# Kernel tuning notes

Hardware: AMD Instinct MI355X
Metric: run time of the kernel (lower is better)

## Reference

```python
import jax, jax.numpy as jnp
import numpy as np

CONTEXT = 256   # context_size
INITIAL = 32    # initial_size
HIDDEN = 256    # hidden_size
WINDOW = 64 - 1 # module stores window_size - 1
TEMP = 50000.0  # soft-argmax temperature
MAX_STEPS = CONTEXT - INITIAL  # cur_pt >= 1 guarantees >=1 index advance per step
B = 4096


def setup_inputs() -> dict:
    key = jax.random.key(0)
    ks = jax.random.split(key, 4)
    def lin_w(k, fan_in, fan_out):
        bound = 1.0 / np.sqrt(fan_in)
        return jax.random.uniform(k, (fan_in, fan_out), jnp.float32, -bound, bound)
    return {
        "x": jax.random.normal(ks[0], (B, CONTEXT), jnp.float32),
        "hid_W": lin_w(ks[1], HIDDEN, HIDDEN),
        "hid_b": jnp.zeros((HIDDEN,), jnp.float32),
        "in_W": lin_w(ks[2], INITIAL, HIDDEN),
        "in_b": jnp.zeros((HIDDEN,), jnp.float32),
        "pred_W": lin_w(ks[3], HIDDEN, WINDOW),
        "pred_b": jnp.zeros((WINDOW,), jnp.float32),
    }


def reference(x, hid_W, hid_b, in_W, in_b, pred_W, pred_b):
    # with per-item active masks. Padded/dense outputs:
    #   pts  [B, MAX_STEPS] : predicted change points (last point dropped, rest zero-padded)
    #   mx   [B, CONTEXT]   : all sigmoid-masked slices scattered back to their positions
    # returned concatenated as [B, MAX_STEPS + CONTEXT].
    Bv = x.shape[0]
    rows = jnp.arange(Bv)[:, None]
    jW = jnp.arange(WINDOW, dtype=jnp.float32)
    iI = jnp.arange(INITIAL)
    iWin = jnp.arange(WINDOW)

    def step(carry, _):
        last, hidden, masked_x, count = carry
        active = last < CONTEXT                       # torch: skip items whose last pt >= context
        last_long = last.astype(jnp.int32)            # floor (last >= INITIAL > 0)
        # slice x[i, last-INITIAL : last]; first step last=INITIAL -> x[:, 0:INITIAL]
        idx = last_long[:, None] - INITIAL + iI       # [B, I]
        slices = jnp.take_along_axis(x, idx, axis=1)
        new_hidden = jnp.tanh(hidden @ hid_W + hid_b + slices @ in_W + in_b)
        hidden = jnp.where(active[:, None], new_hidden, hidden)
        w = new_hidden @ pred_W + pred_b              # [B, WINDOW]
        p = jax.nn.softmax(w * TEMP, axis=-1)
        cur_pt = jnp.minimum(p @ jW + 1.0, float(WINDOW))        # soft-argmax + 1, clamped
        seq_end = jnp.minimum(cur_pt + last, float(CONTEXT))
        seq_end_long = seq_end.astype(jnp.int32)
        # masked slice: mask = 1 - sigmoid(j - cur_pt), j in [0, seq_end_long - last_long)
        pos = last_long[:, None] + iWin                            # [B, WINDOW]
        valid = (pos < seq_end_long[:, None]) & active[:, None]
        mask = 1.0 - jax.nn.sigmoid(jW[None, :] - cur_pt[:, None])
        pos_c = jnp.clip(pos, 0, CONTEXT - 1)
        xg = jnp.take_along_axis(x, pos_c, axis=1)
        contrib = jnp.where(valid, mask * xg, 0.0)
        masked_x = masked_x.at[rows, pos_c].add(contrib)           # segments are disjoint
        last = jnp.where(active, seq_end, last)
        count = count + active.astype(jnp.int32)
        return (last, hidden, masked_x, count), jnp.where(active, seq_end, 0.0)

    init = (jnp.full((Bv,), float(INITIAL), jnp.float32),
            jnp.ones((Bv, HIDDEN), jnp.float32),
            jnp.zeros_like(x),
            jnp.zeros((Bv,), jnp.int32))
    (last, hidden, masked_x, count), ys = jax.lax.scan(step, init, None, length=MAX_STEPS)
    pts = ys.T                                                    # [B, MAX_STEPS]
    keep = jnp.arange(MAX_STEPS)[None, :] < (count - 1)[:, None]  # torch drops last pt per item
    pts = jnp.where(keep, pts, 0.0)
    return jnp.concatenate([pts, masked_x], axis=1)               # [B, MAX_STEPS + CONTEXT]
```

## Files before the change

### kernel.cpp

```cpp
#include <hip/hip_runtime.h>
#include <math.h>


#define CTX     256
#define INIT    32
#define HID     256
#define WIN     63
#define MSTEPS  224
#define OUTROW  (MSTEPS + CTX)
#define IT      4
#define NT      512
#define KSPLIT  112
#define NBLK    512
#define NSLOT   (NBLK * IT)

__global__ void init_counter_kernel(int* cnt, int v) { *cnt = v; }

__global__ void __launch_bounds__(NT)
cpp_kernel(const float* __restrict__ x,
           const float* __restrict__ hid_W,
           const float* __restrict__ hid_b,
           const float* __restrict__ in_W,
           const float* __restrict__ in_b,
           const float* __restrict__ pred_W,
           const float* __restrict__ pred_b,
           float* __restrict__ out,
           int* __restrict__ cnt, int B)
{
    __shared__ double s_x[IT][CTX];
    __shared__ double s_hid[IT][HID];
    __shared__ double s_scr[IT][8][64];
    __shared__ int    s_lastl[IT];
    __shared__ int    s_act[IT];

    const int tid  = threadIdx.x;
    const int lane = tid & 63;
    const int q    = tid >> 6;
    const int j    = tid & (HID - 1);
    const int half = tid >> 8;

    const double bias = (half == 0) ? ((double)hid_b[j] + (double)in_b[j]) : 0.0;
    double* const red = &s_scr[0][0][0];

    int   myitem = -1;
    float mylast = (float)INIT;
    int   sc = 0;

    if (q < IT) {
        const int item = blockIdx.x * IT + q;
        if (item < B) {
            myitem = item;
            float* orow = out + (size_t)item * OUTROW;
            for (int idx = lane; idx < OUTROW; idx += 64) orow[idx] = 0.0f;
            const float4 xv = *(const float4*)&x[(size_t)item * CTX + lane * 4];
            s_x[q][lane * 4 + 0] = (double)xv.x;
            s_x[q][lane * 4 + 1] = (double)xv.y;
            s_x[q][lane * 4 + 2] = (double)xv.z;
            s_x[q][lane * 4 + 3] = (double)xv.w;
            #pragma unroll
            for (int u = 0; u < 4; ++u) s_hid[q][lane + 64 * u] = 1.0;
            if (lane == 0) { s_lastl[q] = INIT; s_act[q] = 1; }
        } else if (lane == 0) { s_lastl[q] = INIT; s_act[q] = 0; }
    }
    __syncthreads();

    for (int iter = 0; iter < (1 << 18); ++iter) {
        int lastl[IT], act[IT];
        #pragma unroll
        for (int it = 0; it < IT; ++it) { lastl[it] = s_lastl[it]; act[it] = s_act[it]; }
        if (!(act[0] | act[1] | act[2] | act[3])) break;

        double acc[IT];
        #pragma unroll
        for (int it = 0; it < IT; ++it) acc[it] = bias;

        if (half == 0) {
            int sb[IT];
            #pragma unroll
            for (int it = 0; it < IT; ++it) {
                int l = lastl[it]; if (l > CTX) l = CTX;
                sb[it] = l - INIT;
            }
            #pragma unroll 4
            for (int m = 0; m < INIT; ++m) {
                const double wv = (double)in_W[m * HID + j];
                #pragma unroll
                for (int it = 0; it < IT; ++it)
                    acc[it] = fma(s_x[it][sb[it] + m], wv, acc[it]);
            }
        }
        {
            const int kbeg = (half == 0) ? 0 : KSPLIT;
            const int kend = (half == 0) ? KSPLIT : HID;
            for (int k = kbeg; k < kend; k += 4) {
                double2 hA[IT], hB[IT];
                #pragma unroll
                for (int it = 0; it < IT; ++it) {
                    hA[it] = *(const double2*)&s_hid[it][k];
                    hB[it] = *(const double2*)&s_hid[it][k + 2];
                }
                const double w0 = (double)hid_W[(size_t)(k + 0) * HID + j];
                const double w1 = (double)hid_W[(size_t)(k + 1) * HID + j];
                const double w2 = (double)hid_W[(size_t)(k + 2) * HID + j];
                const double w3 = (double)hid_W[(size_t)(k + 3) * HID + j];
                #pragma unroll
                for (int it = 0; it < IT; ++it) {
                    acc[it] = fma(hA[it].x, w0, acc[it]);
                    acc[it] = fma(hA[it].y, w1, acc[it]);
                    acc[it] = fma(hB[it].x, w2, acc[it]);
                    acc[it] = fma(hB[it].y, w3, acc[it]);
                }
            }
        }

        if (half == 1) {
            #pragma unroll
            for (int it = 0; it < IT; ++it) red[it * HID + j] = acc[it];
        }
        __syncthreads();

        if (half == 0) {
            #pragma unroll
            for (int it = 0; it < IT; ++it) {
                acc[it] += red[it * HID + j];
                if (act[it]) s_hid[it][j] = (double)tanhf((float)acc[it]);
            }
        }
        __syncthreads();

        double pacc[IT] = {0.0, 0.0, 0.0, 0.0};
        if (lane < WIN) {
            const int kb = q * 32;
            #pragma unroll 4
            for (int kk = 0; kk < 32; ++kk) {
                const int k = kb + kk;
                const double wv = (double)pred_W[k * WIN + lane];
                #pragma unroll
                for (int it = 0; it < IT; ++it)
                    pacc[it] = fma(s_hid[it][k], wv, pacc[it]);
            }
        }
        #pragma unroll
        for (int it = 0; it < IT; ++it) s_scr[it][q][lane] = pacc[it];
        __syncthreads();

        if (q < IT && act[q]) {
            const int it = q;
            float t = -INFINITY;
            if (lane < WIN) {
                const double wv = s_scr[it][0][lane] + s_scr[it][1][lane]
                                + s_scr[it][2][lane] + s_scr[it][3][lane]
                                + s_scr[it][4][lane] + s_scr[it][5][lane]
                                + s_scr[it][6][lane] + s_scr[it][7][lane]
                                + (double)pred_b[lane];
                t = (float)wv * 50000.0f;
            }
            float mx = t;
            #pragma unroll
            for (int off = 32; off > 0; off >>= 1)
                mx = fmaxf(mx, __shfl_xor(mx, off));
            const float e = (lane < WIN) ? expf(t - mx) : 0.0f;
            float S = e;
            #pragma unroll
            for (int off = 32; off > 0; off >>= 1)
                S += __shfl_xor(S, off);
            const float p = e / S;
            float D = p * (float)lane;
            #pragma unroll
            for (int off = 32; off > 0; off >>= 1)
                D += __shfl_xor(D, off);
            float cur = fminf(D + 1.0f, 63.0f);
            float se = fminf(cur + mylast, 256.0f);
            const int sel = (int)se;

            float* orow = out + (size_t)myitem * OUTROW;
            if (lane < WIN) {
                const int pos = lastl[it] + lane;
                if (pos < sel) {
                    const float msk = 1.0f / (1.0f + expf((float)lane - cur));
                    orow[MSTEPS + pos] = msk * (float)s_x[it][pos];
                }
            }
            const bool done = (se >= 256.0f);
            if (lane == 0 && !done) { orow[sc] = se; s_lastl[it] = sel; }
            sc++;
            mylast = se;

            if (done) {
                int nid = 0;
                if (lane == 0) nid = atomicAdd(cnt, 1);
                nid = __shfl(nid, 0);
                if (nid < B) {
                    myitem = nid; mylast = (float)INIT; sc = 0;
                    float* nrow = out + (size_t)nid * OUTROW;
                    for (int idx = lane; idx < OUTROW; idx += 64) nrow[idx] = 0.0f;
                    const float4 xv = *(const float4*)&x[(size_t)nid * CTX + lane * 4];
                    s_x[it][lane * 4 + 0] = (double)xv.x;
                    s_x[it][lane * 4 + 1] = (double)xv.y;
                    s_x[it][lane * 4 + 2] = (double)xv.z;
                    s_x[it][lane * 4 + 3] = (double)xv.w;
                    #pragma unroll
                    for (int u = 0; u < 4; ++u) s_hid[it][lane + 64 * u] = 1.0;
                    if (lane == 0) s_lastl[it] = INIT;
                } else {
                    if (lane == 0) s_act[it] = 0;
                }
            }
        }
        __syncthreads();
    }
}

extern "C" void kernel_launch(void* const* d_in, const int* in_sizes, int n_in,
                              void* d_out, int out_size, void* d_ws, size_t ws_size,
                              hipStream_t stream) {
    const float* x      = (const float*)d_in[0];
    const float* hid_W  = (const float*)d_in[1];
    const float* hid_b  = (const float*)d_in[2];
    const float* in_W   = (const float*)d_in[3];
    const float* in_b   = (const float*)d_in[4];
    const float* pred_W = (const float*)d_in[5];
    const float* pred_b = (const float*)d_in[6];
    float* out = (float*)d_out;
    int*   cnt = (int*)d_ws;

    const int B = in_sizes[0] / CTX;
    init_counter_kernel<<<1, 1, 0, stream>>>(cnt, NSLOT);
    cpp_kernel<<<NBLK, NT, 0, stream>>>(x, hid_W, hid_b, in_W, in_b,
                                        pred_W, pred_b, out, cnt, B);
}
```

Measured before the change: 318.6 us.

## Keep all weights register-resident per thread and halve block count

Each thread now loads its column of in_W/hid_W (144 floats) and its pred_W slice (32 floats) into registers once at kernel start, so weights are no longer re-read from global/L2 on every timestep. The grid is halved to 256 blocks with launch_bounds(…,2), and the x staging store is changed to a strided per-lane pattern. The aim is to remove the per-step weight memory traffic. In exchange it raises register pressure sharply (about 176 floats plus double accumulators), which risks spills or lower occupancy, and fewer blocks means less parallelism across the GPU.

```diff
diff --git a/kernel.cpp b/kernel.cpp
--- a/kernel.cpp
+++ b/kernel.cpp
@@ -10,13 +10,13 @@
 #define OUTROW  (MSTEPS + CTX)
 #define IT      4
 #define NT      512
-#define KSPLIT  112
-#define NBLK    512
+#define KH      112
+#define NBLK    256
 #define NSLOT   (NBLK * IT)
 
 __global__ void init_counter_kernel(int* cnt, int v) { *cnt = v; }
 
-__global__ void __launch_bounds__(NT)
+__global__ void __launch_bounds__(NT, 2)
 cpp_kernel(const float* __restrict__ x,
            const float* __restrict__ hid_W,
            const float* __restrict__ hid_b,
@@ -39,7 +39,25 @@
     const int j    = tid & (HID - 1);
     const int half = tid >> 8;
 
+    float wreg[144];
+    if (half == 0) {
+        #pragma unroll
+        for (int m = 0; m < INIT; ++m) wreg[m] = in_W[m * HID + j];
+        #pragma unroll
+        for (int g = 0; g < KH; ++g)   wreg[INIT + g] = hid_W[(size_t)g * HID + j];
+    } else {
+        #pragma unroll
+        for (int g = 0; g < 144; ++g)  wreg[g] = hid_W[(size_t)(KH + g) * HID + j];
+    }
+    float pwreg[32];
+    {
+        const int kb = q * 32;
+        #pragma unroll
+        for (int kk = 0; kk < 32; ++kk)
+            pwreg[kk] = (lane < WIN) ? pred_W[(kb + kk) * WIN + lane] : 0.0f;
+    }
     const double bias = (half == 0) ? ((double)hid_b[j] + (double)in_b[j]) : 0.0;
+    const float  pbias = (lane < WIN) ? pred_b[lane] : 0.0f;
     double* const red = &s_scr[0][0][0];
 
     int   myitem = -1;
@@ -52,11 +70,9 @@
             myitem = item;
             float* orow = out + (size_t)item * OUTROW;
             for (int idx = lane; idx < OUTROW; idx += 64) orow[idx] = 0.0f;
-            const float4 xv = *(const float4*)&x[(size_t)item * CTX + lane * 4];
-            s_x[q][lane * 4 + 0] = (double)xv.x;
-            s_x[q][lane * 4 + 1] = (double)xv.y;
-            s_x[q][lane * 4 + 2] = (double)xv.z;
-            s_x[q][lane * 4 + 3] = (double)xv.w;
+            #pragma unroll
+            for (int u = 0; u < 4; ++u)
+                s_x[q][lane + 64 * u] = (double)x[(size_t)item * CTX + lane + 64 * u];
             #pragma unroll
             for (int u = 0; u < 4; ++u) s_hid[q][lane + 64 * u] = 1.0;
             if (lane == 0) { s_lastl[q] = INIT; s_act[q] = 1; }
@@ -81,34 +97,34 @@
                 int l = lastl[it]; if (l > CTX) l = CTX;
                 sb[it] = l - INIT;
             }
-            #pragma unroll 4
+            #pragma unroll
             for (int m = 0; m < INIT; ++m) {
-                const double wv = (double)in_W[m * HID + j];
+                const double wv = (double)wreg[m];
                 #pragma unroll
                 for (int it = 0; it < IT; ++it)
                     acc[it] = fma(s_x[it][sb[it] + m], wv, acc[it]);
             }
-        }
-        {
-            const int kbeg = (half == 0) ? 0 : KSPLIT;
-            const int kend = (half == 0) ? KSPLIT : HID;
-            for (int k = kbeg; k < kend; k += 4) {
-                double2 hA[IT], hB[IT];
+            #pragma unroll
+            for (int g = 0; g < KH / 2; ++g) {
+                const double w0 = (double)wreg[INIT + 2 * g];
+                const double w1 = (double)wreg[INIT + 2 * g + 1];
                 #pragma unroll
                 for (int it = 0; it < IT; ++it) {
-                    hA[it] = *(const double2*)&s_hid[it][k];
-                    hB[it] = *(const double2*)&s_hid[it][k + 2];
-                }
-                const double w0 = (double)hid_W[(size_t)(k + 0) * HID + j];
-                const double w1 = (double)hid_W[(size_t)(k + 1) * HID + j];
-                const double w2 = (double)hid_W[(size_t)(k + 2) * HID + j];
-                const double w3 = (double)hid_W[(size_t)(k + 3) * HID + j];
+                    const double2 h = *(const double2*)&s_hid[it][2 * g];
+                    acc[it] = fma(h.x, w0, acc[it]);
+                    acc[it] = fma(h.y, w1, acc[it]);
+                }
+            }
+        } else {
+            #pragma unroll
+            for (int g = 0; g < 72; ++g) {
+                const double w0 = (double)wreg[2 * g];
+                const double w1 = (double)wreg[2 * g + 1];
                 #pragma unroll
                 for (int it = 0; it < IT; ++it) {
-                    acc[it] = fma(hA[it].x, w0, acc[it]);
-                    acc[it] = fma(hA[it].y, w1, acc[it]);
-                    acc[it] = fma(hB[it].x, w2, acc[it]);
-                    acc[it] = fma(hB[it].y, w3, acc[it]);
+                    const double2 h = *(const double2*)&s_hid[it][KH + 2 * g];
+                    acc[it] = fma(h.x, w0, acc[it]);
+                    acc[it] = fma(h.y, w1, acc[it]);
                 }
             }
         }
@@ -129,15 +145,18 @@
         __syncthreads();
 
         double pacc[IT] = {0.0, 0.0, 0.0, 0.0};
-        if (lane < WIN) {
+        {
             const int kb = q * 32;
-            #pragma unroll 4
-            for (int kk = 0; kk < 32; ++kk) {
-                const int k = kb + kk;
-                const double wv = (double)pred_W[k * WIN + lane];
-                #pragma unroll
-                for (int it = 0; it < IT; ++it)
-                    pacc[it] = fma(s_hid[it][k], wv, pacc[it]);
+            #pragma unroll
+            for (int g = 0; g < 16; ++g) {
+                const double w0 = (double)pwreg[2 * g];
+                const double w1 = (double)pwreg[2 * g + 1];
+                #pragma unroll
+                for (int it = 0; it < IT; ++it) {
+                    const double2 h = *(const double2*)&s_hid[it][kb + 2 * g];
+                    pacc[it] = fma(h.x, w0, pacc[it]);
+                    pacc[it] = fma(h.y, w1, pacc[it]);
+                }
             }
         }
         #pragma unroll
@@ -152,7 +171,7 @@
                                 + s_scr[it][2][lane] + s_scr[it][3][lane]
                                 + s_scr[it][4][lane] + s_scr[it][5][lane]
                                 + s_scr[it][6][lane] + s_scr[it][7][lane]
-                                + (double)pred_b[lane];
+                                + (double)pbias;
                 t = (float)wv * 50000.0f;
             }
             float mx = t;
@@ -194,11 +213,9 @@
                     myitem = nid; mylast = (float)INIT; sc = 0;
                     float* nrow = out + (size_t)nid * OUTROW;
                     for (int idx = lane; idx < OUTROW; idx += 64) nrow[idx] = 0.0f;
-                    const float4 xv = *(const float4*)&x[(size_t)nid * CTX + lane * 4];
-                    s_x[it][lane * 4 + 0] = (double)xv.x;
-                    s_x[it][lane * 4 + 1] = (double)xv.y;
-                    s_x[it][lane * 4 + 2] = (double)xv.z;
-                    s_x[it][lane * 4 + 3] = (double)xv.w;
+                    #pragma unroll
+                    for (int u = 0; u < 4; ++u)
+                        s_x[it][lane + 64 * u] = (double)x[(size_t)nid * CTX + lane + 64 * u];
                     #pragma unroll
                     for (int u = 0; u < 4; ++u) s_hid[it][lane + 64 * u] = 1.0;
                     if (lane == 0) s_lastl[it] = INIT;
```

Measured after the change: 1.091 ms. 242% more time.
